# Optimization experiments

Measured on AMD Instinct MI355X. Metric: run time of the kernel, lower is better.

## Reference

```python
import jax, jax.numpy as jnp
import numpy as np

N_NODES = 50000
N_EDGES = 800000
D_IN = 128
D_HID = 128
N_CLS = 47


def setup_inputs() -> dict:
    key = jax.random.key(0)
    ks = jax.random.split(key, 10)
    inp = {
        "features": jax.random.normal(ks[0], (N_NODES, D_IN), dtype=jnp.float32),
        "src": jax.random.randint(ks[1], (N_EDGES,), 0, N_NODES),
        "dst": jax.random.randint(ks[2], (N_EDGES,), 0, N_NODES),
        "Wself0": jax.random.normal(ks[3], (D_IN, D_HID), dtype=jnp.float32) / np.sqrt(D_IN),
        "Wneigh0": jax.random.normal(ks[4], (D_IN, D_HID), dtype=jnp.float32) / np.sqrt(D_IN),
        "b0": jnp.zeros((D_HID,), dtype=jnp.float32),
        "Wself1": jax.random.normal(ks[5], (D_HID, D_HID), dtype=jnp.float32) / np.sqrt(D_HID),
        "Wneigh1": jax.random.normal(ks[6], (D_HID, D_HID), dtype=jnp.float32) / np.sqrt(D_HID),
        "b1": jnp.zeros((D_HID,), dtype=jnp.float32),
        "Wself2": jax.random.normal(ks[7], (D_HID, N_CLS), dtype=jnp.float32) / np.sqrt(D_HID),
        "Wneigh2": jax.random.normal(ks[8], (D_HID, N_CLS), dtype=jnp.float32) / np.sqrt(D_HID),
        "b2": jnp.zeros((N_CLS,), dtype=jnp.float32),
    }
    return inp


def reference(features, src, dst, Wself0, Wneigh0, b0, Wself1, Wneigh1, b1, Wself2, Wneigh2, b2):
    # GraphSAGE (DGL SAGEConv, aggregator_type='mean', eval mode so dropout is identity).
    # Per layer: h_neigh[v] = mean_{(u->v) in E} h[u]; out = h @ W_self + h_neigh @ W_neigh + b
    n = features.shape[0]
    # in-degree for mean aggregation (zero-degree nodes get zero neighbor feature)
    deg = jax.ops.segment_sum(jnp.ones(dst.shape, dtype=features.dtype), dst, num_segments=n)
    inv_deg = (1.0 / jnp.maximum(deg, 1.0))[:, None]  # [N,1]

    def sage_layer(h, Ws, Wn, b, act):
        # gather src features per edge, scatter-add into dst, normalize by in-degree
        agg = jax.ops.segment_sum(h[src], dst, num_segments=n) * inv_deg  # [N, d]
        out = h @ Ws + agg @ Wn + b
        return jax.nn.relu(out) if act else out

    h = sage_layer(features, Wself0, Wneigh0, b0, True)
    h = sage_layer(h, Wself1, Wneigh1, b1, True)
    h = sage_layer(h, Wself2, Wneigh2, b2, False)
    return h
```

## Files before the change

kernel.cpp:

```cpp
#include <hip/hip_runtime.h>

#define D 128
#define NCLS 47
#define CAP 64

typedef short short8 __attribute__((ext_vector_type(8)));
typedef float floatx4 __attribute__((ext_vector_type(4)));
typedef unsigned short ushort8 __attribute__((ext_vector_type(8)));

__device__ __forceinline__ float bf16lo(unsigned int u) {
    union { unsigned int i; float f; } c; c.i = u << 16; return c.f;
}
__device__ __forceinline__ float bf16hi(unsigned int u) {
    union { unsigned int i; float f; } c; c.i = u & 0xffff0000u; return c.f;
}
__device__ __forceinline__ unsigned short f2bf(float f) {
    union { float f; unsigned int i; } c; c.f = f;
    unsigned int r = c.i + 0x7fffu + ((c.i >> 16) & 1u);
    return (unsigned short)(r >> 16);
}
__device__ __forceinline__ unsigned int pack2(float x, float y) {
    return (unsigned int)f2bf(x) | ((unsigned int)f2bf(y) << 16);
}

#define FBm 1024
__global__ __launch_bounds__(256) void fill_prep_kernel(
    const int* __restrict__ src, const int* __restrict__ dst,
    int* __restrict__ cnt, unsigned short* __restrict__ csr, int n_edges,
    const float* __restrict__ f, unsigned int* __restrict__ hA, int npairs, int n,
    const float* __restrict__ Ws0, const float* __restrict__ Wn0, unsigned short* __restrict__ Wt0,
    const float* __restrict__ Ws1, const float* __restrict__ Wn1, unsigned short* __restrict__ Wt1,
    const float* __restrict__ Ws2, const float* __restrict__ Wn2, unsigned short* __restrict__ Wt2) {
    if (blockIdx.x < FBm) {
        int cohort = blockIdx.x & 7;
        int cb = blockIdx.x >> 3;
        int nth = (FBm >> 3) * 256;
        int tid = cb * 256 + threadIdx.x;
        int range = (n + 7) >> 3;
        int lo = cohort * range;
        int hi = lo + range;
        if (hi > n) hi = n;
        for (int e = tid; e < n_edges; e += nth) {
            int d = dst[e];
            if (d >= lo && d < hi) {
                int pos = atomicAdd(&cnt[d], 1);
                if (pos < CAP) csr[d * CAP + pos] = (unsigned short)src[e];
            }
        }
        return;
    }
    int tid = (blockIdx.x - FBm) * 256 + threadIdx.x;
    int stride = (gridDim.x - FBm) * 256;
    int total = npairs + 2 * 128 * 256 + 48 * 256;
    for (int gid = tid; gid < total; gid += stride) {
        if (gid < npairs) {
            float2 v = ((const float2*)f)[gid];
            hA[gid] = pack2(v.x, v.y);
            continue;
        }
        int r = gid - npairs;
        if (r < 128 * 256) {
            int nn = r >> 8, k = r & 255;
            float v = (k < 128) ? Ws0[k * 128 + nn] : Wn0[(k - 128) * 128 + nn];
            Wt0[nn * 256 + k] = f2bf(v);
            continue;
        }
        r -= 128 * 256;
        if (r < 128 * 256) {
            int nn = r >> 8, k = r & 255;
            float v = (k < 128) ? Ws1[k * 128 + nn] : Wn1[(k - 128) * 128 + nn];
            Wt1[nn * 256 + k] = f2bf(v);
            continue;
        }
        r -= 128 * 256;
        if (r < 48 * 256) {
            int nn = r >> 8, k = r & 255;
            float v = 0.0f;
            if (nn < NCLS) v = (k < 128) ? Ws2[k * NCLS + nn] : Wn2[(k - 128) * NCLS + nn];
            Wt2[nn * 256 + k] = f2bf(v);
        }
    }
}

__global__ __launch_bounds__(256) void sage_fused_kernel(
    const unsigned int* __restrict__ hin,
    const unsigned short* __restrict__ csr,
    const int* __restrict__ cnt,
    const unsigned short* __restrict__ Wt,
    const float* __restrict__ bias,
    unsigned short* __restrict__ hout,
    float* __restrict__ out,
    int n, int mode) {
    __shared__ unsigned int selfl[16][68];
    __shared__ unsigned int aggl[16][68];

    int wave = threadIdx.x >> 6;
    int lane = threadIdx.x & 63;
    int base = blockIdx.x * 16;

    for (int i = 0; i < 4; ++i) {
        int li = wave * 4 + i;
        int node = base + li;
        if (node < n) {
            int d = cnt[node];
            if (d > CAP) d = CAP;
            const unsigned short* crow = csr + node * CAP;
            float a0x = 0.f, a0y = 0.f, a1x = 0.f, a1y = 0.f;
            float a2x = 0.f, a2y = 0.f, a3x = 0.f, a3y = 0.f;
            int e = 0;
            for (; e + 8 <= d; e += 8) {
                ushort8 s = *(const ushort8*)(crow + e);
                unsigned int u0 = hin[(size_t)s[0] * 64 + lane];
                unsigned int u1 = hin[(size_t)s[1] * 64 + lane];
                unsigned int u2 = hin[(size_t)s[2] * 64 + lane];
                unsigned int u3 = hin[(size_t)s[3] * 64 + lane];
                unsigned int u4 = hin[(size_t)s[4] * 64 + lane];
                unsigned int u5 = hin[(size_t)s[5] * 64 + lane];
                unsigned int u6 = hin[(size_t)s[6] * 64 + lane];
                unsigned int u7 = hin[(size_t)s[7] * 64 + lane];
                a0x += bf16lo(u0); a0y += bf16hi(u0);
                a1x += bf16lo(u1); a1y += bf16hi(u1);
                a2x += bf16lo(u2); a2y += bf16hi(u2);
                a3x += bf16lo(u3); a3y += bf16hi(u3);
                a0x += bf16lo(u4); a0y += bf16hi(u4);
                a1x += bf16lo(u5); a1y += bf16hi(u5);
                a2x += bf16lo(u6); a2y += bf16hi(u6);
                a3x += bf16lo(u7); a3y += bf16hi(u7);
            }
            for (; e < d; ++e) {
                unsigned int u0 = hin[(size_t)crow[e] * 64 + lane];
                a0x += bf16lo(u0); a0y += bf16hi(u0);
            }
            float inv = 1.0f / fmaxf((float)d, 1.0f);
            float rx = ((a0x + a1x) + (a2x + a3x)) * inv;
            float ry = ((a0y + a1y) + (a2y + a3y)) * inv;
            aggl[li][lane] = pack2(rx, ry);
            selfl[li][lane] = hin[(size_t)node * 64 + lane];
        } else {
            aggl[li][lane] = 0u;
            selfl[li][lane] = 0u;
        }
    }
    __syncthreads();

    int m = lane & 15;
    int quad = lane >> 4;
    int t0 = (mode == 2) ? wave : wave * 2;
    int ntt = (mode == 2) ? ((wave < 3) ? 1 : 0) : 2;
    const unsigned short* arow = (const unsigned short*)&selfl[m][0];
    const unsigned short* lrow = (const unsigned short*)&aggl[m][0];

    floatx4 acc[2];
    acc[0] = (floatx4){0.f, 0.f, 0.f, 0.f};
    acc[1] = (floatx4){0.f, 0.f, 0.f, 0.f};

    if (ntt > 0) {
#pragma unroll
        for (int ko = 0; ko < 128; ko += 32) {
            short8 a = *(const short8*)(arow + ko + quad * 8);
            for (int tt = 0; tt < ntt; ++tt) {
                short8 bfr = *(const short8*)(Wt + (size_t)((t0 + tt) * 16 + m) * 256 + ko + quad * 8);
                acc[tt] = __builtin_amdgcn_mfma_f32_16x16x32_bf16(a, bfr, acc[tt], 0, 0, 0);
            }
        }
#pragma unroll
        for (int ko = 0; ko < 128; ko += 32) {
            short8 a = *(const short8*)(lrow + ko + quad * 8);
            for (int tt = 0; tt < ntt; ++tt) {
                short8 bfr = *(const short8*)(Wt + (size_t)((t0 + tt) * 16 + m) * 256 + 128 + ko + quad * 8);
                acc[tt] = __builtin_amdgcn_mfma_f32_16x16x32_bf16(a, bfr, acc[tt], 0, 0, 0);
            }
        }

        if (mode == 1) {
            for (int tt = 0; tt < ntt; ++tt) {
                int nfeat = (t0 + tt) * 16 + m;
                float bb = bias[nfeat];
#pragma unroll
                for (int r = 0; r < 4; ++r) {
                    int node = base + quad * 4 + r;
                    if (node < n) {
                        float v = fmaxf(acc[tt][r] + bb, 0.0f);
                        hout[(size_t)node * 128 + nfeat] = f2bf(v);
                    }
                }
            }
        } else {
            int nfeat = t0 * 16 + m;
            if (nfeat < NCLS) {
                float bb = bias[nfeat];
#pragma unroll
                for (int r = 0; r < 4; ++r) {
                    int node = base + quad * 4 + r;
                    if (node < n) out[(size_t)node * NCLS + nfeat] = acc[0][r] + bb;
                }
            }
        }
    }
}

extern "C" void kernel_launch(void* const* d_in, const int* in_sizes, int n_in,
                              void* d_out, int out_size, void* d_ws, size_t ws_size,
                              hipStream_t stream) {
    const float* features = (const float*)d_in[0];
    const int* src = (const int*)d_in[1];
    const int* dst = (const int*)d_in[2];
    const float* Ws0 = (const float*)d_in[3];
    const float* Wn0 = (const float*)d_in[4];
    const float* b0 = (const float*)d_in[5];
    const float* Ws1 = (const float*)d_in[6];
    const float* Wn1 = (const float*)d_in[7];
    const float* b1 = (const float*)d_in[8];
    const float* Ws2 = (const float*)d_in[9];
    const float* Wn2 = (const float*)d_in[10];
    const float* b2 = (const float*)d_in[11];
    float* out = (float*)d_out;

    int n = in_sizes[0] / D;
    int n_edges = in_sizes[1];

    int* cnt = (int*)d_ws;
    unsigned short* csr = (unsigned short*)(cnt + 50048);
    unsigned int* hA = (unsigned int*)(csr + (size_t)n * CAP + 32);
    unsigned int* hB = hA + (size_t)n * 64;
    unsigned short* Wt0 = (unsigned short*)(hB + (size_t)n * 64);
    unsigned short* Wt1 = Wt0 + 128 * 256;
    unsigned short* Wt2 = Wt1 + 128 * 256;

    int npairs = n * 64;

    hipMemsetAsync(cnt, 0, (size_t)n * sizeof(int), stream);
    fill_prep_kernel<<<2048, 256, 0, stream>>>(
        src, dst, cnt, csr, n_edges, features, hA, npairs, n,
        Ws0, Wn0, Wt0, Ws1, Wn1, Wt1, Ws2, Wn2, Wt2);

    int tiles = (n + 15) / 16;

    sage_fused_kernel<<<tiles, 256, 0, stream>>>(hA, csr, cnt, Wt0, b0,
                                                 (unsigned short*)hB, nullptr, n, 1);
    sage_fused_kernel<<<tiles, 256, 0, stream>>>(hB, csr, cnt, Wt1, b1,
                                                 (unsigned short*)hA, nullptr, n, 1);
    sage_fused_kernel<<<tiles, 256, 0, stream>>>(hA, csr, cnt, Wt2, b2,
                                                 nullptr, out, n, 2);
}
```

Measured before the change: 334.0 us.

## Vectorize neighbor gather with 16B loads across four edge groups per wave

The mean-aggregation gather is reorganized so that each wave splits into four 16-lane groups. Each group handles a different edge, and each lane loads 16 bytes (8 bf16 features) instead of 4. Partial sums are then combined with cross-lane shuffles. Self-feature rows are staged into shared memory with one uint4 load per thread, and the CSR fill loop reads dst as int4 to cut load instructions. The intent is fewer, wider memory transactions with more gathers in flight per wave, at the cost of shuffle reductions and more per-lane registers.

```diff
diff --git a/kernel.cpp b/kernel.cpp
--- a/kernel.cpp
+++ b/kernel.cpp
@@ -21,6 +21,13 @@
 }
 __device__ __forceinline__ unsigned int pack2(float x, float y) {
     return (unsigned int)f2bf(x) | ((unsigned int)f2bf(y) << 16);
+}
+
+__device__ __forceinline__ void acc8(uint4 u, float* a) {
+    a[0] += bf16lo(u.x); a[1] += bf16hi(u.x);
+    a[2] += bf16lo(u.y); a[3] += bf16hi(u.y);
+    a[4] += bf16lo(u.z); a[5] += bf16hi(u.z);
+    a[6] += bf16lo(u.w); a[7] += bf16hi(u.w);
 }
 
 #define FBm 1024
@@ -40,11 +47,33 @@
         int lo = cohort * range;
         int hi = lo + range;
         if (hi > n) hi = n;
-        for (int e = tid; e < n_edges; e += nth) {
+        const int4* dst4 = (const int4*)dst;
+        int nq = n_edges >> 2;
+        for (int q = tid; q < nq; q += nth) {
+            int4 dd = dst4[q];
+            int e = q << 2;
+            if (dd.x >= lo && dd.x < hi) {
+                int p = atomicAdd(&cnt[dd.x], 1);
+                if (p < CAP) csr[dd.x * CAP + p] = (unsigned short)src[e];
+            }
+            if (dd.y >= lo && dd.y < hi) {
+                int p = atomicAdd(&cnt[dd.y], 1);
+                if (p < CAP) csr[dd.y * CAP + p] = (unsigned short)src[e + 1];
+            }
+            if (dd.z >= lo && dd.z < hi) {
+                int p = atomicAdd(&cnt[dd.z], 1);
+                if (p < CAP) csr[dd.z * CAP + p] = (unsigned short)src[e + 2];
+            }
+            if (dd.w >= lo && dd.w < hi) {
+                int p = atomicAdd(&cnt[dd.w], 1);
+                if (p < CAP) csr[dd.w * CAP + p] = (unsigned short)src[e + 3];
+            }
+        }
+        for (int e = (nq << 2) + tid; e < n_edges; e += nth) {
             int d = dst[e];
             if (d >= lo && d < hi) {
-                int pos = atomicAdd(&cnt[d], 1);
-                if (pos < CAP) csr[d * CAP + pos] = (unsigned short)src[e];
+                int p = atomicAdd(&cnt[d], 1);
+                if (p < CAP) csr[d * CAP + p] = (unsigned short)src[e];
             }
         }
         return;
@@ -97,6 +126,19 @@
     int wave = threadIdx.x >> 6;
     int lane = threadIdx.x & 63;
     int base = blockIdx.x * 16;
+    const uint4* hin4 = (const uint4*)hin;
+
+    {
+        int rowi = threadIdx.x >> 4;
+        int cq = threadIdx.x & 15;
+        int ns = base + rowi;
+        uint4 sv; sv.x = 0u; sv.y = 0u; sv.z = 0u; sv.w = 0u;
+        if (ns < n) sv = hin4[(size_t)ns * 16 + cq];
+        *(uint4*)&selfl[rowi][cq * 4] = sv;
+    }
+
+    int g = lane >> 4;
+    int fl = lane & 15;
 
     for (int i = 0; i < 4; ++i) {
         int li = wave * 4 + i;
@@ -105,40 +147,56 @@
             int d = cnt[node];
             if (d > CAP) d = CAP;
             const unsigned short* crow = csr + node * CAP;
-            float a0x = 0.f, a0y = 0.f, a1x = 0.f, a1y = 0.f;
-            float a2x = 0.f, a2y = 0.f, a3x = 0.f, a3y = 0.f;
+            float a[8];
+#pragma unroll
+            for (int j = 0; j < 8; ++j) a[j] = 0.0f;
             int e = 0;
-            for (; e + 8 <= d; e += 8) {
-                ushort8 s = *(const ushort8*)(crow + e);
-                unsigned int u0 = hin[(size_t)s[0] * 64 + lane];
-                unsigned int u1 = hin[(size_t)s[1] * 64 + lane];
-                unsigned int u2 = hin[(size_t)s[2] * 64 + lane];
-                unsigned int u3 = hin[(size_t)s[3] * 64 + lane];
-                unsigned int u4 = hin[(size_t)s[4] * 64 + lane];
-                unsigned int u5 = hin[(size_t)s[5] * 64 + lane];
-                unsigned int u6 = hin[(size_t)s[6] * 64 + lane];
-                unsigned int u7 = hin[(size_t)s[7] * 64 + lane];
-                a0x += bf16lo(u0); a0y += bf16hi(u0);
-                a1x += bf16lo(u1); a1y += bf16hi(u1);
-                a2x += bf16lo(u2); a2y += bf16hi(u2);
-                a3x += bf16lo(u3); a3y += bf16hi(u3);
-                a0x += bf16lo(u4); a0y += bf16hi(u4);
-                a1x += bf16lo(u5); a1y += bf16hi(u5);
-                a2x += bf16lo(u6); a2y += bf16hi(u6);
-                a3x += bf16lo(u7); a3y += bf16hi(u7);
-            }
-            for (; e < d; ++e) {
-                unsigned int u0 = hin[(size_t)crow[e] * 64 + lane];
-                a0x += bf16lo(u0); a0y += bf16hi(u0);
-            }
-            float inv = 1.0f / fmaxf((float)d, 1.0f);
-            float rx = ((a0x + a1x) + (a2x + a3x)) * inv;
-            float ry = ((a0y + a1y) + (a2y + a3y)) * inv;
-            aggl[li][lane] = pack2(rx, ry);
-            selfl[li][lane] = hin[(size_t)node * 64 + lane];
-        } else {
-            aggl[li][lane] = 0u;
-            selfl[li][lane] = 0u;
+            for (; e + 16 <= d; e += 16) {
+                int i0 = crow[e + g];
+                int i1 = crow[e + 4 + g];
+                int i2 = crow[e + 8 + g];
+                int i3 = crow[e + 12 + g];
+                uint4 u0 = hin4[(size_t)i0 * 16 + fl];
+                uint4 u1 = hin4[(size_t)i1 * 16 + fl];
+                uint4 u2 = hin4[(size_t)i2 * 16 + fl];
+                uint4 u3 = hin4[(size_t)i3 * 16 + fl];
+                acc8(u0, a); acc8(u1, a); acc8(u2, a); acc8(u3, a);
+            }
+            if (e + 8 <= d) {
+                int i0 = crow[e + g];
+                int i1 = crow[e + 4 + g];
+                uint4 u0 = hin4[(size_t)i0 * 16 + fl];
+                uint4 u1 = hin4[(size_t)i1 * 16 + fl];
+                acc8(u0, a); acc8(u1, a);
+                e += 8;
+            }
+            for (; e < d; e += 4) {
+                int ee = e + g;
+                bool v = ee < d;
+                int idx = crow[v ? ee : e];
+                uint4 u = hin4[(size_t)idx * 16 + fl];
+                if (!v) { u.x = 0u; u.y = 0u; u.z = 0u; u.w = 0u; }
+                acc8(u, a);
+            }
+#pragma unroll
+            for (int j = 0; j < 8; ++j) {
+                float v = a[j];
+                v += __shfl_xor(v, 16, 64);
+                v += __shfl_xor(v, 32, 64);
+                a[j] = v;
+            }
+            if (g == 0) {
+                float inv = 1.0f / fmaxf((float)d, 1.0f);
+                uint4 o;
+                o.x = pack2(a[0] * inv, a[1] * inv);
+                o.y = pack2(a[2] * inv, a[3] * inv);
+                o.z = pack2(a[4] * inv, a[5] * inv);
+                o.w = pack2(a[6] * inv, a[7] * inv);
+                *(uint4*)&aggl[li][fl * 4] = o;
+            }
+        } else if (g == 0) {
+            uint4 z; z.x = 0u; z.y = 0u; z.z = 0u; z.w = 0u;
+            *(uint4*)&aggl[li][fl * 4] = z;
         }
     }
     __syncthreads();
```

Measured after the change: 307.2 us. 1.09x faster.
